# Kernel optimization log

Hardware: AMD Instinct MI355X
Metric: run time of the kernel (lower is better)

## Reference

```python
import jax, jax.numpy as jnp
import numpy as np

B, N, E, C = 1, 100000, 1600000, 128


def setup_inputs() -> dict:
    key = jax.random.key(0)
    k1, k2, k3, k4 = jax.random.split(key, 4)
    x = jax.random.normal(k1, (B, N, C), dtype=jnp.float32)
    edge_index = jax.random.randint(k2, (2, E), 0, N, dtype=jnp.int32)
    W_2 = jax.random.normal(k3, (C,), dtype=jnp.float32)
    W_3 = jax.random.normal(k4, (C,), dtype=jnp.float32)
    return {"x": x, "edge_index": edge_index, "W_2": W_2, "W_3": W_3}


def reference(x, edge_index, W_2, W_3):
    # x: [B, N, C]; edge_index: [2, E] (src, dst)
    src, dst = edge_index[0], edge_index[1]
    num_nodes = x.shape[1]
    # per-edge attention weight: w[b,e] = <(x*W_3)[b,src_e], x[b,dst_e]>
    x3 = (x * W_3)[:, src, :]          # [B, E, C] gather
    x4 = x[:, dst, :]                  # [B, E, C] gather
    w = jnp.einsum('bec,bec->be', x3, x4)  # [B, E]
    # value messages with diagonal W_2 scaling, scattered to destination nodes.
    # Equivalent to out = einsum('bij,bih->bjh', dense_adj(w), x*W_2),
    # where dense_adj[src,dst] = w (to_dense_adj sums duplicate edges; so does segment_sum).
    x2 = x * W_2                       # [B, N, C]
    msg = w[..., None] * x2[:, src, :]  # [B, E, C]
    out = jax.vmap(lambda m: jax.ops.segment_sum(m, dst, num_segments=num_nodes))(msg)
    return out  # [B, N, C]
```

## Files before the change

### kernel.cpp

```cpp
#include <hip/hip_runtime.h>
#include <hip/hip_fp16.h>


#define CCH 128
#define BSHIFT 5
#define BWIDTH 32
#define MAXBIN 4096
#define CH 8192
#define LDSCAP 1280
#define SCAN_BLOCK 256
#define SCAN_ITEMS 4
#define SCAN_TILE (SCAN_BLOCK * SCAN_ITEMS)


__global__ __launch_bounds__(256) void k_pack_hist(
    const float* __restrict__ x, __half* __restrict__ xh, int n4, int nPack,
    const int* __restrict__ dst, int E, int NBIN, int* __restrict__ hist_bm)
{
    __shared__ int cnt[MAXBIN];
    const int tid = threadIdx.x;

    if (blockIdx.x < nPack) {
        const int i = blockIdx.x * 256 + tid;
        if (i < n4) {
            float4 v = reinterpret_cast<const float4*>(x)[i];
            __half2* o = reinterpret_cast<__half2*>(xh) + (size_t)i * 2;
            o[0] = __floats2half2_rn(v.x, v.y);
            o[1] = __floats2half2_rn(v.z, v.w);
        }
        return;
    }

    const int blk = blockIdx.x - nPack;
    for (int b = tid; b < NBIN; b += 256) cnt[b] = 0;
    __syncthreads();

    const int e0 = blk * CH;
    #pragma unroll
    for (int k = 0; k < CH / 1024; ++k) {
        const int g = (e0 >> 2) + k * 256 + tid;
        const int e = g << 2;
        if (e >= E) continue;
        if (e + 4 <= E) {
            const int4 d4 = reinterpret_cast<const int4*>(dst)[g];
            atomicAdd(&cnt[d4.x >> BSHIFT], 1);
            atomicAdd(&cnt[d4.y >> BSHIFT], 1);
            atomicAdd(&cnt[d4.z >> BSHIFT], 1);
            atomicAdd(&cnt[d4.w >> BSHIFT], 1);
        } else {
            for (int ee = e; ee < E; ++ee) atomicAdd(&cnt[dst[ee] >> BSHIFT], 1);
        }
    }
    __syncthreads();
    int* hb = hist_bm + (size_t)blk * NBIN;
    for (int b = tid; b < NBIN; b += 256) hb[b] = cnt[b];
}


__global__ void k_pscan1(const int* __restrict__ hist_bm, int M, int NBIN, int NBLK,
                         int* __restrict__ partial, int* __restrict__ blocksum) {
    __shared__ int sdata[SCAN_BLOCK];
    const int base = blockIdx.x * SCAN_TILE;
    const int t = threadIdx.x;
    int v[SCAN_ITEMS];
    int local = 0;
    #pragma unroll
    for (int k = 0; k < SCAN_ITEMS; ++k) {
        int idx = base + t * SCAN_ITEMS + k;
        int val = 0;
        if (idx < M) {
            int bin = idx / NBLK, blk = idx % NBLK;
            val = hist_bm[(size_t)blk * NBIN + bin];
        }
        v[k] = val;
        local += val;
    }
    sdata[t] = local;
    __syncthreads();
    #pragma unroll
    for (int off = 1; off < SCAN_BLOCK; off <<= 1) {
        int val = (t >= off) ? sdata[t - off] : 0;
        __syncthreads();
        sdata[t] += val;
        __syncthreads();
    }
    const int incl = sdata[t];
    int run = incl - local;
    if (t == SCAN_BLOCK - 1) blocksum[blockIdx.x] = incl;
    #pragma unroll
    for (int k = 0; k < SCAN_ITEMS; ++k) {
        int idx = base + t * SCAN_ITEMS + k;
        if (idx < M) partial[idx] = run;
        run += v[k];
    }
}

__global__ void k_scan2(int* __restrict__ blocksum, int nb) {
    __shared__ int sdata[1024];
    const int t = threadIdx.x;
    const int v = (t < nb) ? blocksum[t] : 0;
    sdata[t] = v;
    __syncthreads();
    for (int off = 1; off < 1024; off <<= 1) {
        int val = (t >= off) ? sdata[t - off] : 0;
        __syncthreads();
        sdata[t] += val;
        __syncthreads();
    }
    if (t < nb) blocksum[t] = sdata[t] - v;
}


__global__ __launch_bounds__(256) void k_place(
    const int* __restrict__ src, const int* __restrict__ dst, int E, int NBIN, int NBLK,
    const int* __restrict__ partial, const int* __restrict__ blocksum,
    unsigned int* __restrict__ coarse)
{
    __shared__ int lcur[MAXBIN];
    const int blk = blockIdx.x;
    const int tid = threadIdx.x;
    for (int b = tid; b < NBIN; b += 256) {
        const size_t idx = (size_t)b * NBLK + blk;
        lcur[b] = partial[idx] + blocksum[idx / SCAN_TILE];
    }
    __syncthreads();

    const int e0 = blk * CH;
    #pragma unroll
    for (int k = 0; k < CH / 1024; ++k) {
        const int g = (e0 >> 2) + k * 256 + tid;
        const int e = g << 2;
        if (e >= E) continue;
        if (e + 4 <= E) {
            const int4 d4 = reinterpret_cast<const int4*>(dst)[g];
            const int4 s4 = reinterpret_cast<const int4*>(src)[g];
            int p;
            p = atomicAdd(&lcur[d4.x >> BSHIFT], 1);
            coarse[p] = (unsigned)s4.x | ((unsigned)(d4.x & (BWIDTH - 1)) << 17);
            p = atomicAdd(&lcur[d4.y >> BSHIFT], 1);
            coarse[p] = (unsigned)s4.y | ((unsigned)(d4.y & (BWIDTH - 1)) << 17);
            p = atomicAdd(&lcur[d4.z >> BSHIFT], 1);
            coarse[p] = (unsigned)s4.z | ((unsigned)(d4.z & (BWIDTH - 1)) << 17);
            p = atomicAdd(&lcur[d4.w >> BSHIFT], 1);
            coarse[p] = (unsigned)s4.w | ((unsigned)(d4.w & (BWIDTH - 1)) << 17);
        } else {
            for (int ee = e; ee < E; ++ee) {
                const int d = dst[ee], s = src[ee];
                int p = atomicAdd(&lcur[d >> BSHIFT], 1);
                coarse[p] = (unsigned)s | ((unsigned)(d & (BWIDTH - 1)) << 17);
            }
        }
    }
}


__global__ __launch_bounds__(256) void k_sort_accum(
    const __half* __restrict__ xh,
    const float* __restrict__ W2,
    const float* __restrict__ W3,
    const unsigned int* __restrict__ coarse,
    const int* __restrict__ partial, const int* __restrict__ blocksum,
    int NBIN, int NBLK, int E, int N,
    float* __restrict__ out)
{
    __shared__ unsigned int raw[LDSCAP];
    __shared__ int srcl[LDSCAP];
    __shared__ int cnt[BWIDTH], offs[BWIDTH], cur[BWIDTH];

    const int bin = blockIdx.x;
    const int tid = threadIdx.x;
    const size_t i0 = (size_t)bin * NBLK;
    const int beg = partial[i0] + blocksum[i0 / SCAN_TILE];
    const int end = (bin + 1 < NBIN)
        ? partial[i0 + NBLK] + blocksum[(i0 + NBLK) / SCAN_TILE] : E;
    const int mtot = end - beg;
    const int m = (mtot < LDSCAP) ? mtot : LDSCAP;

    if (tid < BWIDTH) cnt[tid] = 0;
    __syncthreads();

    for (int i = tid; i < m; i += 256) {
        unsigned u = coarse[beg + i];
        raw[i] = u;
        atomicAdd(&cnt[u >> 17], 1);
    }
    __syncthreads();

    if (tid < BWIDTH) {
        int c = cnt[tid];
        int v = c;
        #pragma unroll
        for (int d2 = 1; d2 < BWIDTH; d2 <<= 1) {
            int t2 = __shfl_up(v, d2, 64);
            if (tid >= d2) v += t2;
        }
        offs[tid] = v - c;
        cur[tid]  = v - c;
    }
    __syncthreads();

    for (int i = tid; i < m; i += 256) {
        unsigned u = raw[i];
        int p = atomicAdd(&cur[u >> 17], 1);
        srcl[p] = (int)(u & 0x1FFFFu);
    }
    __syncthreads();

    const int w    = tid >> 6;
    const int lane = tid & 63;
    const int grp  = lane >> 4;
    const int sl   = lane & 15;

    const float4 w3a = *reinterpret_cast<const float4*>(W3 + sl * 8);
    const float4 w3b = *reinterpret_cast<const float4*>(W3 + sl * 8 + 4);
    const float4 w2a = *reinterpret_cast<const float4*>(W2 + sl * 8);
    const float4 w2b = *reinterpret_cast<const float4*>(W2 + sl * 8 + 4);

    const char* xb = (const char*)xh;
    const int choff = sl << 4;

    for (int i = 0; i < BWIDTH / 4; ++i) {
        const int dl = w * (BWIDTH / 4) + i;
        const int node = (bin << BSHIFT) + dl;
        if (node >= N) break;

        union { int4 i4; __half2 h[4]; } uD;
        uD.i4 = *reinterpret_cast<const int4*>(xb + (((size_t)node) << 8) + choff);
        const float2 e0 = __half22float2(uD.h[0]);
        const float2 e1 = __half22float2(uD.h[1]);
        const float2 e2 = __half22float2(uD.h[2]);
        const float2 e3 = __half22float2(uD.h[3]);
        const float4 va = make_float4(w3a.x * e0.x, w3a.y * e0.y, w3a.z * e1.x, w3a.w * e1.y);
        const float4 vb = make_float4(w3b.x * e2.x, w3b.y * e2.y, w3b.z * e3.x, w3b.w * e3.y);

        float4 accA = make_float4(0.f, 0.f, 0.f, 0.f);
        float4 accB = make_float4(0.f, 0.f, 0.f, 0.f);

        const int b0 = offs[dl];
        const int c  = cnt[dl];

        int j = 0;
        for (; j + 8 <= c; j += 8) {
            const int sA = srcl[b0 + j + grp];
            const int sB = srcl[b0 + j + 4 + grp];
            union { int4 i4; __half2 h[4]; } uA, uB;
            uA.i4 = *reinterpret_cast<const int4*>(xb + (((size_t)sA) << 8) + choff);
            uB.i4 = *reinterpret_cast<const int4*>(xb + (((size_t)sB) << 8) + choff);
            const float2 fA0 = __half22float2(uA.h[0]);
            const float2 fA1 = __half22float2(uA.h[1]);
            const float2 fA2 = __half22float2(uA.h[2]);
            const float2 fA3 = __half22float2(uA.h[3]);
            const float2 fB0 = __half22float2(uB.h[0]);
            const float2 fB1 = __half22float2(uB.h[1]);
            const float2 fB2 = __half22float2(uB.h[2]);
            const float2 fB3 = __half22float2(uB.h[3]);
            float pA = fA0.x * va.x + fA0.y * va.y + fA1.x * va.z + fA1.y * va.w
                     + fA2.x * vb.x + fA2.y * vb.y + fA3.x * vb.z + fA3.y * vb.w;
            float pB = fB0.x * va.x + fB0.y * va.y + fB1.x * va.z + fB1.y * va.w
                     + fB2.x * vb.x + fB2.y * vb.y + fB3.x * vb.z + fB3.y * vb.w;
            #pragma unroll
            for (int off = 1; off < 16; off <<= 1) {
                pA += __shfl_xor(pA, off, 64);
                pB += __shfl_xor(pB, off, 64);
            }
            accA.x += pA * fA0.x + pB * fB0.x;
            accA.y += pA * fA0.y + pB * fB0.y;
            accA.z += pA * fA1.x + pB * fB1.x;
            accA.w += pA * fA1.y + pB * fB1.y;
            accB.x += pA * fA2.x + pB * fB2.x;
            accB.y += pA * fA2.y + pB * fB2.y;
            accB.z += pA * fA3.x + pB * fB3.x;
            accB.w += pA * fA3.y + pB * fB3.y;
        }
        for (; j < c; j += 4) {
            const bool ok = (j + grp) < c;
            const int s0 = ok ? srcl[b0 + j + grp] : srcl[b0];
            union { int4 i4; __half2 h[4]; } u0;
            u0.i4 = *reinterpret_cast<const int4*>(xb + (((size_t)s0) << 8) + choff);
            const float2 f0 = __half22float2(u0.h[0]);
            const float2 f1 = __half22float2(u0.h[1]);
            const float2 f2 = __half22float2(u0.h[2]);
            const float2 f3 = __half22float2(u0.h[3]);
            float p = f0.x * va.x + f0.y * va.y + f1.x * va.z + f1.y * va.w
                    + f2.x * vb.x + f2.y * vb.y + f3.x * vb.z + f3.y * vb.w;
            if (!ok) p = 0.f;
            #pragma unroll
            for (int off = 1; off < 16; off <<= 1) p += __shfl_xor(p, off, 64);
            accA.x += p * f0.x;
            accA.y += p * f0.y;
            accA.z += p * f1.x;
            accA.w += p * f1.y;
            accB.x += p * f2.x;
            accB.y += p * f2.y;
            accB.z += p * f3.x;
            accB.w += p * f3.y;
        }
        for (int i2 = LDSCAP; i2 < mtot; ++i2) {
            const unsigned u = coarse[beg + i2];
            if ((int)(u >> 17) != dl) continue;
            const int s0 = (int)(u & 0x1FFFFu);
            union { int4 i4; __half2 h[4]; } u0;
            u0.i4 = *reinterpret_cast<const int4*>(xb + (((size_t)s0) << 8) + choff);
            const float2 f0 = __half22float2(u0.h[0]);
            const float2 f1 = __half22float2(u0.h[1]);
            const float2 f2 = __half22float2(u0.h[2]);
            const float2 f3 = __half22float2(u0.h[3]);
            float p = f0.x * va.x + f0.y * va.y + f1.x * va.z + f1.y * va.w
                    + f2.x * vb.x + f2.y * vb.y + f3.x * vb.z + f3.y * vb.w;
            #pragma unroll
            for (int off = 1; off < 16; off <<= 1) p += __shfl_xor(p, off, 64);
            if (grp != 0) p = 0.f;
            accA.x += p * f0.x;
            accA.y += p * f0.y;
            accA.z += p * f1.x;
            accA.w += p * f1.y;
            accB.x += p * f2.x;
            accB.y += p * f2.y;
            accB.z += p * f3.x;
            accB.w += p * f3.y;
        }

        #pragma unroll
        for (int off = 16; off < 64; off <<= 1) {
            accA.x += __shfl_xor(accA.x, off, 64);
            accA.y += __shfl_xor(accA.y, off, 64);
            accA.z += __shfl_xor(accA.z, off, 64);
            accA.w += __shfl_xor(accA.w, off, 64);
            accB.x += __shfl_xor(accB.x, off, 64);
            accB.y += __shfl_xor(accB.y, off, 64);
            accB.z += __shfl_xor(accB.z, off, 64);
            accB.w += __shfl_xor(accB.w, off, 64);
        }

        accA.x *= w2a.x; accA.y *= w2a.y; accA.z *= w2a.z; accA.w *= w2a.w;
        accB.x *= w2b.x; accB.y *= w2b.y; accB.z *= w2b.z; accB.w *= w2b.w;
        const float av[8] = {accA.x, accA.y, accA.z, accA.w, accB.x, accB.y, accB.z, accB.w};
        float2 st = make_float2(av[2 * grp], av[2 * grp + 1]);
        *reinterpret_cast<float2*>(out + (size_t)node * CCH + sl * 8 + 2 * grp) = st;
    }
}


__global__ __launch_bounds__(256) void edge_gather_scatter(
    const float* __restrict__ x, const int* __restrict__ edge_index,
    const float* __restrict__ W2, const float* __restrict__ W3,
    float* __restrict__ out, int E)
{
    const int e    = (blockIdx.x * blockDim.x + threadIdx.x) >> 6;
    const int lane = threadIdx.x & 63;
    if (e >= E) return;
    const int s = edge_index[e];
    const int d = edge_index[E + e];
    const float2 xs = *reinterpret_cast<const float2*>(x + (size_t)s * CCH + lane * 2);
    const float2 xd = *reinterpret_cast<const float2*>(x + (size_t)d * CCH + lane * 2);
    const float2 w3 = *reinterpret_cast<const float2*>(W3 + lane * 2);
    const float2 w2 = *reinterpret_cast<const float2*>(W2 + lane * 2);
    float p = xs.x * w3.x * xd.x + xs.y * w3.y * xd.y;
    #pragma unroll
    for (int off = 32; off > 0; off >>= 1) p += __shfl_xor(p, off, 64);
    float* o = out + (size_t)d * CCH + lane * 2;
    atomicAdd(o,     p * xs.x * w2.x);
    atomicAdd(o + 1, p * xs.y * w2.y);
}


extern "C" void kernel_launch(void* const* d_in, const int* in_sizes, int n_in,
                              void* d_out, int out_size, void* d_ws, size_t ws_size,
                              hipStream_t stream) {
    const float* x          = (const float*)d_in[0];
    const int*   edge_index = (const int*)  d_in[1];
    const float* W2         = (const float*)d_in[2];
    const float* W3         = (const float*)d_in[3];
    float*       out        = (float*)d_out;

    const int E = in_sizes[1] / 2;
    const int N = out_size / CCH;
    const int* src = edge_index;
    const int* dst = edge_index + E;

    const int NBIN = (N + BWIDTH - 1) >> BSHIFT;
    const int NBLK = (E + CH - 1) / CH;
    const long long Mll = (long long)NBIN * NBLK;
    const int M = (int)Mll;
    const int nb1 = (M + SCAN_TILE - 1) / SCAN_TILE;

    const size_t xh_bytes = (size_t)N * CCH * 2;
    const size_t need = xh_bytes + (size_t)E * 4 + 2 * (size_t)M * 4 + 1024 * 4;

    const bool aligned16 = (((uintptr_t)src & 15) == 0) && (((uintptr_t)dst & 15) == 0);

    if (N <= (1 << 17) && NBIN <= MAXBIN && Mll <= (1LL << 20) && nb1 <= 1024 &&
        aligned16 && ws_size >= need) {
        char* base = (char*)d_ws;
        __half* xh       = (__half*)base;        base += xh_bytes;
        unsigned* coarse = (unsigned*)base;      base += (size_t)E * 4;
        int* hist_bm     = (int*)base;           base += (size_t)M * 4;
        int* partial     = (int*)base;           base += (size_t)M * 4;
        int* blocksum    = (int*)base;

        const int n4 = N * CCH / 4;
        const int nPack = (n4 + 255) / 256;

        k_pack_hist<<<nPack + NBLK, 256, 0, stream>>>(x, xh, n4, nPack,
                                                      dst, E, NBIN, hist_bm);
        k_pscan1<<<nb1, SCAN_BLOCK, 0, stream>>>(hist_bm, M, NBIN, NBLK, partial, blocksum);
        k_scan2<<<1, 1024, 0, stream>>>(blocksum, nb1);
        k_place<<<NBLK, 256, 0, stream>>>(src, dst, E, NBIN, NBLK,
                                          partial, blocksum, coarse);
        k_sort_accum<<<NBIN, 256, 0, stream>>>(xh, W2, W3, coarse,
                                               partial, blocksum,
                                               NBIN, NBLK, E, N, out);
        return;
    }

    hipMemsetAsync(d_out, 0, (size_t)out_size * sizeof(float), stream);
    const int grid = (E * 64 + 255) / 256;
    edge_gather_scatter<<<grid, 256, 0, stream>>>(x, edge_index, W2, W3, out, E);
}
```

Before: 147.5 us.

## Assign one destination node per 16-lane group instead of per wavefront

Work is remapped so that each 16-lane group in a wavefront owns its own destination node, where previously all four groups of a wave split one node's edges. This removes the cross-group shuffle reduction of the accumulators at the end of each node and lets each lane write full float4 outputs. The inner loop is unrolled to four independent source gathers per iteration to keep memory-level parallelism up. In exchange, lanes in the same wave now run different edge counts, so uneven degrees cause divergence, and register pressure rises from the 4-way unroll.

```diff
diff --git a/kernel.cpp b/kernel.cpp
--- a/kernel.cpp
+++ b/kernel.cpp
@@ -206,10 +206,10 @@
     }
     __syncthreads();
 
-    const int w    = tid >> 6;
     const int lane = tid & 63;
     const int grp  = lane >> 4;
     const int sl   = lane & 15;
+    const int gid  = (tid >> 6) * 4 + grp;
 
     const float4 w3a = *reinterpret_cast<const float4*>(W3 + sl * 8);
     const float4 w3b = *reinterpret_cast<const float4*>(W3 + sl * 8 + 4);
@@ -219,124 +219,130 @@
     const char* xb = (const char*)xh;
     const int choff = sl << 4;
 
-    for (int i = 0; i < BWIDTH / 4; ++i) {
-        const int dl = w * (BWIDTH / 4) + i;
+    #pragma unroll
+    for (int i = 0; i < BWIDTH / 16; ++i) {
+        const int dl = gid * (BWIDTH / 16) + i;
         const int node = (bin << BSHIFT) + dl;
-        if (node >= N) break;
-
-        union { int4 i4; __half2 h[4]; } uD;
-        uD.i4 = *reinterpret_cast<const int4*>(xb + (((size_t)node) << 8) + choff);
-        const float2 e0 = __half22float2(uD.h[0]);
-        const float2 e1 = __half22float2(uD.h[1]);
-        const float2 e2 = __half22float2(uD.h[2]);
-        const float2 e3 = __half22float2(uD.h[3]);
-        const float4 va = make_float4(w3a.x * e0.x, w3a.y * e0.y, w3a.z * e1.x, w3a.w * e1.y);
-        const float4 vb = make_float4(w3b.x * e2.x, w3b.y * e2.y, w3b.z * e3.x, w3b.w * e3.y);
-
-        float4 accA = make_float4(0.f, 0.f, 0.f, 0.f);
-        float4 accB = make_float4(0.f, 0.f, 0.f, 0.f);
-
-        const int b0 = offs[dl];
-        const int c  = cnt[dl];
-
-        int j = 0;
-        for (; j + 8 <= c; j += 8) {
-            const int sA = srcl[b0 + j + grp];
-            const int sB = srcl[b0 + j + 4 + grp];
-            union { int4 i4; __half2 h[4]; } uA, uB;
-            uA.i4 = *reinterpret_cast<const int4*>(xb + (((size_t)sA) << 8) + choff);
-            uB.i4 = *reinterpret_cast<const int4*>(xb + (((size_t)sB) << 8) + choff);
-            const float2 fA0 = __half22float2(uA.h[0]);
-            const float2 fA1 = __half22float2(uA.h[1]);
-            const float2 fA2 = __half22float2(uA.h[2]);
-            const float2 fA3 = __half22float2(uA.h[3]);
-            const float2 fB0 = __half22float2(uB.h[0]);
-            const float2 fB1 = __half22float2(uB.h[1]);
-            const float2 fB2 = __half22float2(uB.h[2]);
-            const float2 fB3 = __half22float2(uB.h[3]);
-            float pA = fA0.x * va.x + fA0.y * va.y + fA1.x * va.z + fA1.y * va.w
-                     + fA2.x * vb.x + fA2.y * vb.y + fA3.x * vb.z + fA3.y * vb.w;
-            float pB = fB0.x * va.x + fB0.y * va.y + fB1.x * va.z + fB1.y * va.w
-                     + fB2.x * vb.x + fB2.y * vb.y + fB3.x * vb.z + fB3.y * vb.w;
-            #pragma unroll
-            for (int off = 1; off < 16; off <<= 1) {
-                pA += __shfl_xor(pA, off, 64);
-                pB += __shfl_xor(pB, off, 64);
+        if (node < N) {
+            union { int4 i4; __half2 h[4]; } uD;
+            uD.i4 = *reinterpret_cast<const int4*>(xb + (((size_t)node) << 8) + choff);
+            const float2 e0 = __half22float2(uD.h[0]);
+            const float2 e1 = __half22float2(uD.h[1]);
+            const float2 e2 = __half22float2(uD.h[2]);
+            const float2 e3 = __half22float2(uD.h[3]);
+            const float4 va = make_float4(w3a.x * e0.x, w3a.y * e0.y,
+                                          w3a.z * e1.x, w3a.w * e1.y);
+            const float4 vb = make_float4(w3b.x * e2.x, w3b.y * e2.y,
+                                          w3b.z * e3.x, w3b.w * e3.y);
+
+            float4 accA = make_float4(0.f, 0.f, 0.f, 0.f);
+            float4 accB = make_float4(0.f, 0.f, 0.f, 0.f);
+
+            const int b0 = offs[dl];
+            const int c  = cnt[dl];
+
+            int j = 0;
+            for (; j + 4 <= c; j += 4) {
+                const int s0 = srcl[b0 + j];
+                const int s1 = srcl[b0 + j + 1];
+                const int s2 = srcl[b0 + j + 2];
+                const int s3 = srcl[b0 + j + 3];
+                union { int4 i4; __half2 h[4]; } u0, u1, u2, u3;
+                u0.i4 = *reinterpret_cast<const int4*>(xb + (((size_t)s0) << 8) + choff);
+                u1.i4 = *reinterpret_cast<const int4*>(xb + (((size_t)s1) << 8) + choff);
+                u2.i4 = *reinterpret_cast<const int4*>(xb + (((size_t)s2) << 8) + choff);
+                u3.i4 = *reinterpret_cast<const int4*>(xb + (((size_t)s3) << 8) + choff);
+                const float2 f00 = __half22float2(u0.h[0]);
+                const float2 f01 = __half22float2(u0.h[1]);
+                const float2 f02 = __half22float2(u0.h[2]);
+                const float2 f03 = __half22float2(u0.h[3]);
+                const float2 f10 = __half22float2(u1.h[0]);
+                const float2 f11 = __half22float2(u1.h[1]);
+                const float2 f12 = __half22float2(u1.h[2]);
+                const float2 f13 = __half22float2(u1.h[3]);
+                const float2 f20 = __half22float2(u2.h[0]);
+                const float2 f21 = __half22float2(u2.h[1]);
+                const float2 f22 = __half22float2(u2.h[2]);
+                const float2 f23 = __half22float2(u2.h[3]);
+                const float2 f30 = __half22float2(u3.h[0]);
+                const float2 f31 = __half22float2(u3.h[1]);
+                const float2 f32 = __half22float2(u3.h[2]);
+                const float2 f33 = __half22float2(u3.h[3]);
+                float p0 = f00.x * va.x + f00.y * va.y + f01.x * va.z + f01.y * va.w
+                         + f02.x * vb.x + f02.y * vb.y + f03.x * vb.z + f03.y * vb.w;
+                float p1 = f10.x * va.x + f10.y * va.y + f11.x * va.z + f11.y * va.w
+                         + f12.x * vb.x + f12.y * vb.y + f13.x * vb.z + f13.y * vb.w;
+                float p2 = f20.x * va.x + f20.y * va.y + f21.x * va.z + f21.y * va.w
+                         + f22.x * vb.x + f22.y * vb.y + f23.x * vb.z + f23.y * vb.w;
+                float p3 = f30.x * va.x + f30.y * va.y + f31.x * va.z + f31.y * va.w
+                         + f32.x * vb.x + f32.y * vb.y + f33.x * vb.z + f33.y * vb.w;
+                #pragma unroll
+                for (int off = 1; off < 16; off <<= 1) {
+                    p0 += __shfl_xor(p0, off, 64);
+                    p1 += __shfl_xor(p1, off, 64);
+                    p2 += __shfl_xor(p2, off, 64);
+                    p3 += __shfl_xor(p3, off, 64);
+                }
+                accA.x += p0 * f00.x + p1 * f10.x + p2 * f20.x + p3 * f30.x;
+                accA.y += p0 * f00.y + p1 * f10.y + p2 * f20.y + p3 * f30.y;
+                accA.z += p0 * f01.x + p1 * f11.x + p2 * f21.x + p3 * f31.x;
+                accA.w += p0 * f01.y + p1 * f11.y + p2 * f21.y + p3 * f31.y;
+                accB.x += p0 * f02.x + p1 * f12.x + p2 * f22.x + p3 * f32.x;
+                accB.y += p0 * f02.y + p1 * f12.y + p2 * f22.y + p3 * f32.y;
+                accB.z += p0 * f03.x + p1 * f13.x + p2 * f23.x + p3 * f33.x;
+                accB.w += p0 * f03.y + p1 * f13.y + p2 * f23.y + p3 * f33.y;
             }
-            accA.x += pA * fA0.x + pB * fB0.x;
-            accA.y += pA * fA0.y + pB * fB0.y;
-            accA.z += pA * fA1.x + pB * fB1.x;
-            accA.w += pA * fA1.y + pB * fB1.y;
-            accB.x += pA * fA2.x + pB * fB2.x;
-            accB.y += pA * fA2.y + pB * fB2.y;
-            accB.z += pA * fA3.x + pB * fB3.x;
-            accB.w += pA * fA3.y + pB * fB3.y;
-        }
-        for (; j < c; j += 4) {
-            const bool ok = (j + grp) < c;
-            const int s0 = ok ? srcl[b0 + j + grp] : srcl[b0];
-            union { int4 i4; __half2 h[4]; } u0;
-            u0.i4 = *reinterpret_cast<const int4*>(xb + (((size_t)s0) << 8) + choff);
-            const float2 f0 = __half22float2(u0.h[0]);
-            const float2 f1 = __half22float2(u0.h[1]);
-            const float2 f2 = __half22float2(u0.h[2]);
-            const float2 f3 = __half22float2(u0.h[3]);
-            float p = f0.x * va.x + f0.y * va.y + f1.x * va.z + f1.y * va.w
-                    + f2.x * vb.x + f2.y * vb.y + f3.x * vb.z + f3.y * vb.w;
-            if (!ok) p = 0.f;
-            #pragma unroll
-            for (int off = 1; off < 16; off <<= 1) p += __shfl_xor(p, off, 64);
-            accA.x += p * f0.x;
-            accA.y += p * f0.y;
-            accA.z += p * f1.x;
-            accA.w += p * f1.y;
-            accB.x += p * f2.x;
-            accB.y += p * f2.y;
-            accB.z += p * f3.x;
-            accB.w += p * f3.y;
-        }
-        for (int i2 = LDSCAP; i2 < mtot; ++i2) {
-            const unsigned u = coarse[beg + i2];
-            if ((int)(u >> 17) != dl) continue;
-            const int s0 = (int)(u & 0x1FFFFu);
-            union { int4 i4; __half2 h[4]; } u0;
-            u0.i4 = *reinterpret_cast<const int4*>(xb + (((size_t)s0) << 8) + choff);
-            const float2 f0 = __half22float2(u0.h[0]);
-            const float2 f1 = __half22float2(u0.h[1]);
-            const float2 f2 = __half22float2(u0.h[2]);
-            const float2 f3 = __half22float2(u0.h[3]);
-            float p = f0.x * va.x + f0.y * va.y + f1.x * va.z + f1.y * va.w
-                    + f2.x * vb.x + f2.y * vb.y + f3.x * vb.z + f3.y * vb.w;
-            #pragma unroll
-            for (int off = 1; off < 16; off <<= 1) p += __shfl_xor(p, off, 64);
-            if (grp != 0) p = 0.f;
-            accA.x += p * f0.x;
-            accA.y += p * f0.y;
-            accA.z += p * f1.x;
-            accA.w += p * f1.y;
-            accB.x += p * f2.x;
-            accB.y += p * f2.y;
-            accB.z += p * f3.x;
-            accB.w += p * f3.y;
-        }
-
-        #pragma unroll
-        for (int off = 16; off < 64; off <<= 1) {
-            accA.x += __shfl_xor(accA.x, off, 64);
-            accA.y += __shfl_xor(accA.y, off, 64);
-            accA.z += __shfl_xor(accA.z, off, 64);
-            accA.w += __shfl_xor(accA.w, off, 64);
-            accB.x += __shfl_xor(accB.x, off, 64);
-            accB.y += __shfl_xor(accB.y, off, 64);
-            accB.z += __shfl_xor(accB.z, off, 64);
-            accB.w += __shfl_xor(accB.w, off, 64);
-        }
-
-        accA.x *= w2a.x; accA.y *= w2a.y; accA.z *= w2a.z; accA.w *= w2a.w;
-        accB.x *= w2b.x; accB.y *= w2b.y; accB.z *= w2b.z; accB.w *= w2b.w;
-        const float av[8] = {accA.x, accA.y, accA.z, accA.w, accB.x, accB.y, accB.z, accB.w};
-        float2 st = make_float2(av[2 * grp], av[2 * grp + 1]);
-        *reinterpret_cast<float2*>(out + (size_t)node * CCH + sl * 8 + 2 * grp) = st;
+            for (; j < c; ++j) {
+                const int s0 = srcl[b0 + j];
+                union { int4 i4; __half2 h[4]; } u0;
+                u0.i4 = *reinterpret_cast<const int4*>(xb + (((size_t)s0) << 8) + choff);
+                const float2 f0 = __half22float2(u0.h[0]);
+                const float2 f1 = __half22float2(u0.h[1]);
+                const float2 f2 = __half22float2(u0.h[2]);
+                const float2 f3 = __half22float2(u0.h[3]);
+                float p = f0.x * va.x + f0.y * va.y + f1.x * va.z + f1.y * va.w
+                        + f2.x * vb.x + f2.y * vb.y + f3.x * vb.z + f3.y * vb.w;
+                #pragma unroll
+                for (int off = 1; off < 16; off <<= 1) p += __shfl_xor(p, off, 64);
+                accA.x += p * f0.x;
+                accA.y += p * f0.y;
+                accA.z += p * f1.x;
+                accA.w += p * f1.y;
+                accB.x += p * f2.x;
+                accB.y += p * f2.y;
+                accB.z += p * f3.x;
+                accB.w += p * f3.y;
+            }
+            for (int i2 = LDSCAP; i2 < mtot; ++i2) {
+                const unsigned u = coarse[beg + i2];
+                if ((int)(u >> 17) != dl) continue;
+                const int s0 = (int)(u & 0x1FFFFu);
+                union { int4 i4; __half2 h[4]; } u0;
+                u0.i4 = *reinterpret_cast<const int4*>(xb + (((size_t)s0) << 8) + choff);
+                const float2 f0 = __half22float2(u0.h[0]);
+                const float2 f1 = __half22float2(u0.h[1]);
+                const float2 f2 = __half22float2(u0.h[2]);
+                const float2 f3 = __half22float2(u0.h[3]);
+                float p = f0.x * va.x + f0.y * va.y + f1.x * va.z + f1.y * va.w
+                        + f2.x * vb.x + f2.y * vb.y + f3.x * vb.z + f3.y * vb.w;
+                #pragma unroll
+                for (int off = 1; off < 16; off <<= 1) p += __shfl_xor(p, off, 64);
+                accA.x += p * f0.x;
+                accA.y += p * f0.y;
+                accA.z += p * f1.x;
+                accA.w += p * f1.y;
+                accB.x += p * f2.x;
+                accB.y += p * f2.y;
+                accB.z += p * f3.x;
+                accB.w += p * f3.y;
+            }
+
+            accA.x *= w2a.x; accA.y *= w2a.y; accA.z *= w2a.z; accA.w *= w2a.w;
+            accB.x *= w2b.x; accB.y *= w2b.y; accB.z *= w2b.z; accB.w *= w2b.w;
+            float* orow = out + (size_t)node * CCH + sl * 8;
+            *reinterpret_cast<float4*>(orow)     = accA;
+            *reinterpret_cast<float4*>(orow + 4) = accB;
+        }
     }
 }
 
```

Result: faster. 125.5 us (-14.9%).
